# Optimization experiments

Hardware: AMD Instinct MI355X
Metric: run time of the kernel (lower is better)

Reference implementation:

```python
import jax, jax.numpy as jnp
import numpy as np

# Synthetic NEAT-style layered DAG (matches init_kwargs)
N_IN = 512      # input nodes
L = 5           # computed layers (last = outputs)
M = 2048        # nodes per computed layer
FAN = 32        # incoming edges per computed node
B = 1024        # batch size
N = N_IN + L * M        # total nodes
E = M * FAN             # edges per layer (grouped by destination layer)


def setup_inputs() -> dict:
    rng = np.random.default_rng(0)
    src = np.zeros((L, E), np.int32)
    dst = np.zeros((L, E), np.int32)
    for l in range(L):
        prefix = N_IN + l * M  # edges may come from any earlier node (DAG w/ skips)
        src[l] = rng.integers(0, prefix, size=E)
        dst[l] = np.repeat(np.arange(M, dtype=np.int32), FAN)
    key = jax.random.key(0)
    k1, k2, k3 = jax.random.split(key, 3)
    x = jax.random.normal(k1, (B, N_IN), jnp.float32)
    weights = jax.random.normal(k2, (L, E), jnp.float32) * 0.1
    biases = jax.random.normal(k3, (L, M), jnp.float32) * 0.01
    return {
        "x": x,
        "weights": weights,
        "biases": biases,
        "src_idx": jnp.asarray(src),
        "dst_idx": jnp.asarray(dst),
    }


def reference(x, weights, biases, src_idx, dst_idx):
    b = x.shape[0]
    # values[:, node] as in the torch module; inputs copied in first
    vals = jnp.zeros((b, N), x.dtype).at[:, :N_IN].set(x)
    for l in range(L):  # topological layers (fixed, small count)
        # gather source activations for this layer's edges and weight them
        contrib = vals[:, src_idx[l]] * weights[l]                    # [B, E]
        # scatter-add into destination nodes of this layer
        layer = jnp.zeros((b, M), x.dtype).at[:, dst_idx[l]].add(contrib)
        layer = jax.nn.relu(layer + biases[l])
        vals = vals.at[:, N_IN + l * M : N_IN + (l + 1) * M].set(layer)
    # output nodes = last computed layer
    return vals[:, N_IN + (L - 1) * M :]
```

## Files before the change

### kernel.cpp

```cpp
#include <hip/hip_runtime.h>

#define N_IN    512
#define NLAYERS 5
#define M_NODES 2048
#define FAN     32
#define B_BATCH 1024
#define E_EDGES (M_NODES * FAN)
#define N_TOTAL (N_IN + NLAYERS * M_NODES)
#define PREFIX4 (N_IN + 4 * M_NODES)

#define CB      4
#define NBLK    (B_BATCH / CB)
#define GROUPS  (M_NODES / 64)
#define ECH     (FAN / 4)
#define NODES_ALL (NLAYERS * M_NODES)

typedef unsigned short u16;
typedef unsigned int   u32;

__device__ __forceinline__ u16 f2bf(float f) {
    u32 b = __float_as_uint(f);
    return (u16)((b + 0x7FFFu + ((b >> 16) & 1u)) >> 16);
}

__global__ __launch_bounds__(256) void pack_edges(
    const float* __restrict__ w,
    const int* __restrict__ src,
    u32* __restrict__ pck) {
    const int n = blockIdx.x * 256 + threadIdx.x;
    if (n >= NODES_ALL) return;
    const int l = n >> 11;
    const int j = n & (M_NODES - 1);

    u32 words[FAN];
    int cnt[16];
#pragma unroll
    for (int i = 0; i < 16; ++i) cnt[i] = 0;

    const size_t eb = (size_t)l * E_EDGES + (size_t)j * FAN;
#pragma unroll 1
    for (int k = 0; k < FAN; ++k) {
        const int s = src[eb + k];
        words[k] = ((u32)f2bf(w[eb + k]) << 16) | (u32)(s & 0xFFFF);
        cnt[s & 15]++;
    }
    int startp[16];
    int acc = 0;
#pragma unroll
    for (int i = 0; i < 16; ++i) { startp[i] = acc; acc += cnt[i]; }

    const int g    = j >> 6;
    const int lane = j & 63;
    const int rot  = j & 31;
    const size_t nb = (size_t)(l * GROUPS + g) * ECH;
#pragma unroll 1
    for (int k = 0; k < FAN; ++k) {
        const u32 wd  = words[k];
        const int key = wd & 15;
        const int r   = startp[key]++;
        const int kp  = (r + rot) & 31;
        pck[((nb + (kp >> 2)) * 64 + lane) * 4 + (kp & 3)] = wd;
    }
}

__global__ __launch_bounds__(1024) void net_kernel(
    const float* __restrict__ x,
    const u32* __restrict__ pck,
    const float* __restrict__ bias,
    float* __restrict__ out) {
    __shared__ uint2 vals2[PREFIX4];

    const int t   = threadIdx.x;
    const int blk = blockIdx.x;

    if (t < N_IN) {
        const float v0 = x[(size_t)(CB * blk + 0) * N_IN + t];
        const float v1 = x[(size_t)(CB * blk + 1) * N_IN + t];
        const float v2 = x[(size_t)(CB * blk + 2) * N_IN + t];
        const float v3 = x[(size_t)(CB * blk + 3) * N_IN + t];
        vals2[t] = make_uint2((u32)f2bf(v0) | ((u32)f2bf(v1) << 16),
                              (u32)f2bf(v2) | ((u32)f2bf(v3) << 16));
    }

    for (int l = 0; l < NLAYERS; ++l) {
        __syncthreads();
        const int base = N_IN + l * M_NODES;
#pragma unroll
        for (int r = 0; r < 2; ++r) {
            const int j     = r * 1024 + t;
            const int g     = j >> 6;
            const int lane6 = j & 63;
            const uint4* ep = reinterpret_cast<const uint4*>(pck) +
                              (size_t)(l * GROUPS + g) * ECH * 64 + lane6;
            const float bj = bias[l * M_NODES + j];
            float a0 = bj, a1 = bj, a2 = bj, a3 = bj;

            uint4 wd = ep[0];
#pragma unroll
            for (int ec = 0; ec < ECH; ++ec) {
                const uint4 nxt = (ec < ECH - 1) ? ep[(ec + 1) * 64] : wd;
#pragma unroll
                for (int c = 0; c < 4; ++c) {
                    const u32 word = (c == 0) ? wd.x : (c == 1) ? wd.y
                                    : (c == 2) ? wd.z : wd.w;
                    const u32 s    = word & 0xFFFFu;
                    const float wv = __uint_as_float(word & 0xFFFF0000u);
                    const uint2 v  = vals2[s];
                    a0 = fmaf(wv, __uint_as_float(v.x << 16),          a0);
                    a1 = fmaf(wv, __uint_as_float(v.x & 0xFFFF0000u), a1);
                    a2 = fmaf(wv, __uint_as_float(v.y << 16),          a2);
                    a3 = fmaf(wv, __uint_as_float(v.y & 0xFFFF0000u), a3);
                }
                wd = nxt;
            }
            a0 = fmaxf(a0, 0.f);
            a1 = fmaxf(a1, 0.f);
            a2 = fmaxf(a2, 0.f);
            a3 = fmaxf(a3, 0.f);
            if (l < NLAYERS - 1) {
                vals2[base + j] =
                    make_uint2((u32)f2bf(a0) | ((u32)f2bf(a1) << 16),
                               (u32)f2bf(a2) | ((u32)f2bf(a3) << 16));
            } else {
                out[(size_t)(CB * blk + 0) * M_NODES + j] = a0;
                out[(size_t)(CB * blk + 1) * M_NODES + j] = a1;
                out[(size_t)(CB * blk + 2) * M_NODES + j] = a2;
                out[(size_t)(CB * blk + 3) * M_NODES + j] = a3;
            }
        }
    }
}

extern "C" void kernel_launch(void* const* d_in, const int* in_sizes, int n_in,
                              void* d_out, int out_size, void* d_ws, size_t ws_size,
                              hipStream_t stream) {
    const float* x       = (const float*)d_in[0];
    const float* weights = (const float*)d_in[1];
    const float* biases  = (const float*)d_in[2];
    const int*   src_idx = (const int*)d_in[3];
    float* out = (float*)d_out;
    u32*   pck = (u32*)d_ws;

    pack_edges<<<(NODES_ALL + 255) / 256, 256, 0, stream>>>(
        weights, src_idx, pck);

    net_kernel<<<NBLK, 1024, 0, stream>>>(x, pck, biases, out);
}
```

Before: 107.0 us.

## Rewrite edge packing as block-cooperative shared-memory sort with coalesced I/O

The edge-packing kernel now uses one 1024-thread block per 64-node group. Threads read src and weight pairs with coalesced vector loads, bucket them by source low bits using shared-memory atomics, and write the packed output fully coalesced. The old version had each thread walk its own node's 32 edges with strided loads and scattered stores. The change targets the memory inefficiency of the preprocessing kernel, at the cost of extra barriers and shared atomics. Because atomic order is nondeterministic, the ordering within each bucket may vary from run to run, but the sums stay equivalent.

```diff
diff --git a/kernel.cpp b/kernel.cpp
--- a/kernel.cpp
+++ b/kernel.cpp
@@ -23,43 +23,59 @@
     return (u16)((b + 0x7FFFu + ((b >> 16) & 1u)) >> 16);
 }
 
-__global__ __launch_bounds__(256) void pack_edges(
+__global__ __launch_bounds__(1024) void pack_edges(
     const float* __restrict__ w,
     const int* __restrict__ src,
     u32* __restrict__ pck) {
-    const int n = blockIdx.x * 256 + threadIdx.x;
-    if (n >= NODES_ALL) return;
-    const int l = n >> 11;
-    const int j = n & (M_NODES - 1);
+    __shared__ u32 s_word[2048];
+    __shared__ u32 s_sorted[64][32];
+    __shared__ int s_cnt[64][16];
+    __shared__ int s_start[64][16];
 
-    u32 words[FAN];
-    int cnt[16];
+    const int t  = threadIdx.x;
+    const int lg = blockIdx.x;
+    const size_t ebase = (size_t)lg * 2048;
+
+    if (t < 64 * 16) ((int*)s_cnt)[t] = 0;
+    __syncthreads();
+
+    const int e0 = t * 2;
+    const int node = e0 >> 5;
+    const int2   s2 = *reinterpret_cast<const int2*>(src + ebase + e0);
+    const float2 w2 = *reinterpret_cast<const float2*>(w + ebase + e0);
+    const u32 wd0 = ((u32)f2bf(w2.x) << 16) | (u32)(s2.x & 0xFFFF);
+    const u32 wd1 = ((u32)f2bf(w2.y) << 16) | (u32)(s2.y & 0xFFFF);
+    s_word[e0]     = wd0;
+    s_word[e0 + 1] = wd1;
+    atomicAdd(&s_cnt[node][s2.x & 15], 1);
+    atomicAdd(&s_cnt[node][s2.y & 15], 1);
+    __syncthreads();
+
+    if (t < 64) {
+        int acc = 0;
 #pragma unroll
-    for (int i = 0; i < 16; ++i) cnt[i] = 0;
+        for (int i = 0; i < 16; ++i) {
+            s_start[t][i] = acc;
+            acc += s_cnt[t][i];
+        }
+    }
+    __syncthreads();
 
-    const size_t eb = (size_t)l * E_EDGES + (size_t)j * FAN;
-#pragma unroll 1
-    for (int k = 0; k < FAN; ++k) {
-        const int s = src[eb + k];
-        words[k] = ((u32)f2bf(w[eb + k]) << 16) | (u32)(s & 0xFFFF);
-        cnt[s & 15]++;
+    const int rot = node & 31;
+    {
+        const int r0 = atomicAdd(&s_start[node][wd0 & 15], 1);
+        s_sorted[node][(r0 + rot) & 31] = wd0;
+        const int r1 = atomicAdd(&s_start[node][wd1 & 15], 1);
+        s_sorted[node][(r1 + rot) & 31] = wd1;
     }
-    int startp[16];
-    int acc = 0;
+    __syncthreads();
+
 #pragma unroll
-    for (int i = 0; i < 16; ++i) { startp[i] = acc; acc += cnt[i]; }
-
-    const int g    = j >> 6;
-    const int lane = j & 63;
-    const int rot  = j & 31;
-    const size_t nb = (size_t)(l * GROUPS + g) * ECH;
-#pragma unroll 1
-    for (int k = 0; k < FAN; ++k) {
-        const u32 wd  = words[k];
-        const int key = wd & 15;
-        const int r   = startp[key]++;
-        const int kp  = (r + rot) & 31;
-        pck[((nb + (kp >> 2)) * 64 + lane) * 4 + (kp & 3)] = wd;
+    for (int i = 0; i < 2; ++i) {
+        const int p    = t + i * 1024;
+        const int lane = (p >> 2) & 63;
+        const int kp   = ((p >> 8) << 2) | (p & 3);
+        pck[ebase + p] = s_sorted[lane][kp];
     }
 }
 
@@ -141,8 +157,7 @@
     float* out = (float*)d_out;
     u32*   pck = (u32*)d_ws;
 
-    pack_edges<<<(NODES_ALL + 255) / 256, 256, 0, stream>>>(
-        weights, src_idx, pck);
+    pack_edges<<<NLAYERS * GROUPS, 1024, 0, stream>>>(weights, src_idx, pck);
 
     net_kernel<<<NBLK, 1024, 0, stream>>>(x, pck, biases, out);
 }
```

Measured after the change: 90.32 us. -15.6%, faster.

## Parallelize edge packing per edge, use packed FMA and batched LDS gathers

Applied to the files above, without the earlier changes.

The pack kernel now gives each edge its own thread instead of looping per node, and it drops the bank-conflict-avoiding sort and rotation of edges by source low bits. The main kernel issues all four LDS gathers of a chunk before the FMAs. It also uses two-wide float vector FMAs, which can map to packed FP32 instructions on CDNA3/4. The aim is to cut the serial pack cost and the ALU instruction count, but removing the bank-aware ordering may bring back LDS bank conflicts in the gather.

```diff
diff --git a/kernel.cpp b/kernel.cpp
--- a/kernel.cpp
+++ b/kernel.cpp
@@ -13,54 +13,30 @@
 #define NBLK    (B_BATCH / CB)
 #define GROUPS  (M_NODES / 64)
 #define ECH     (FAN / 4)
-#define NODES_ALL (NLAYERS * M_NODES)
 
 typedef unsigned short u16;
 typedef unsigned int   u32;
+typedef __attribute__((ext_vector_type(2))) float f32x2;
 
 __device__ __forceinline__ u16 f2bf(float f) {
     u32 b = __float_as_uint(f);
     return (u16)((b + 0x7FFFu + ((b >> 16) & 1u)) >> 16);
 }
 
-__global__ __launch_bounds__(256) void pack_edges(
+__global__ __launch_bounds__(1024) void pack_edges(
     const float* __restrict__ w,
     const int* __restrict__ src,
     u32* __restrict__ pck) {
-    const int n = blockIdx.x * 256 + threadIdx.x;
-    if (n >= NODES_ALL) return;
-    const int l = n >> 11;
-    const int j = n & (M_NODES - 1);
-
-    u32 words[FAN];
-    int cnt[16];
-#pragma unroll
-    for (int i = 0; i < 16; ++i) cnt[i] = 0;
-
-    const size_t eb = (size_t)l * E_EDGES + (size_t)j * FAN;
-#pragma unroll 1
-    for (int k = 0; k < FAN; ++k) {
-        const int s = src[eb + k];
-        words[k] = ((u32)f2bf(w[eb + k]) << 16) | (u32)(s & 0xFFFF);
-        cnt[s & 15]++;
-    }
-    int startp[16];
-    int acc = 0;
-#pragma unroll
-    for (int i = 0; i < 16; ++i) { startp[i] = acc; acc += cnt[i]; }
-
+    const int e = blockIdx.x * 1024 + threadIdx.x;
+    const int l    = e >> 16;
+    const int j    = (e >> 5) & (M_NODES - 1);
+    const int k    = e & (FAN - 1);
     const int g    = j >> 6;
     const int lane = j & 63;
-    const int rot  = j & 31;
-    const size_t nb = (size_t)(l * GROUPS + g) * ECH;
-#pragma unroll 1
-    for (int k = 0; k < FAN; ++k) {
-        const u32 wd  = words[k];
-        const int key = wd & 15;
-        const int r   = startp[key]++;
-        const int kp  = (r + rot) & 31;
-        pck[((nb + (kp >> 2)) * 64 + lane) * 4 + (kp & 3)] = wd;
-    }
+    const int ec   = k >> 2;
+    const int c    = k & 3;
+    const u32 word = ((u32)f2bf(w[e]) << 16) | (u32)(src[e] & 0xFFFF);
+    pck[((((l * GROUPS + g) * ECH + ec) * 64) + lane) * 4 + c] = word;
 }
 
 __global__ __launch_bounds__(1024) void net_kernel(
@@ -82,41 +58,47 @@
                               (u32)f2bf(v2) | ((u32)f2bf(v3) << 16));
     }
 
+    const int g0    = t >> 6;
+    const int lane6 = t & 63;
+
     for (int l = 0; l < NLAYERS; ++l) {
         __syncthreads();
         const int base = N_IN + l * M_NODES;
 #pragma unroll
         for (int r = 0; r < 2; ++r) {
-            const int j     = r * 1024 + t;
-            const int g     = j >> 6;
-            const int lane6 = j & 63;
+            const int j = r * 1024 + t;
             const uint4* ep = reinterpret_cast<const uint4*>(pck) +
-                              (size_t)(l * GROUPS + g) * ECH * 64 + lane6;
+                              (size_t)(l * GROUPS + g0 + r * 16) * ECH * 64 +
+                              lane6;
             const float bj = bias[l * M_NODES + j];
-            float a0 = bj, a1 = bj, a2 = bj, a3 = bj;
+            f32x2 a01 = {bj, bj};
+            f32x2 a23 = {bj, bj};
 
             uint4 wd = ep[0];
 #pragma unroll
             for (int ec = 0; ec < ECH; ++ec) {
                 const uint4 nxt = (ec < ECH - 1) ? ep[(ec + 1) * 64] : wd;
+                const u32 ew[4] = {wd.x, wd.y, wd.z, wd.w};
+                uint2 v[4];
+#pragma unroll
+                for (int c = 0; c < 4; ++c) v[c] = vals2[ew[c] & 0xFFFFu];
 #pragma unroll
                 for (int c = 0; c < 4; ++c) {
-                    const u32 word = (c == 0) ? wd.x : (c == 1) ? wd.y
-                                    : (c == 2) ? wd.z : wd.w;
-                    const u32 s    = word & 0xFFFFu;
-                    const float wv = __uint_as_float(word & 0xFFFF0000u);
-                    const uint2 v  = vals2[s];
-                    a0 = fmaf(wv, __uint_as_float(v.x << 16),          a0);
-                    a1 = fmaf(wv, __uint_as_float(v.x & 0xFFFF0000u), a1);
-                    a2 = fmaf(wv, __uint_as_float(v.y << 16),          a2);
-                    a3 = fmaf(wv, __uint_as_float(v.y & 0xFFFF0000u), a3);
+                    const float wv = __uint_as_float(ew[c] & 0xFFFF0000u);
+                    const f32x2 w2 = {wv, wv};
+                    const f32x2 p01 = {__uint_as_float(v[c].x << 16),
+                                       __uint_as_float(v[c].x & 0xFFFF0000u)};
+                    const f32x2 p23 = {__uint_as_float(v[c].y << 16),
+                                       __uint_as_float(v[c].y & 0xFFFF0000u)};
+                    a01 = __builtin_elementwise_fma(w2, p01, a01);
+                    a23 = __builtin_elementwise_fma(w2, p23, a23);
                 }
                 wd = nxt;
             }
-            a0 = fmaxf(a0, 0.f);
-            a1 = fmaxf(a1, 0.f);
-            a2 = fmaxf(a2, 0.f);
-            a3 = fmaxf(a3, 0.f);
+            const float a0 = fmaxf(a01[0], 0.f);
+            const float a1 = fmaxf(a01[1], 0.f);
+            const float a2 = fmaxf(a23[0], 0.f);
+            const float a3 = fmaxf(a23[1], 0.f);
             if (l < NLAYERS - 1) {
                 vals2[base + j] =
                     make_uint2((u32)f2bf(a0) | ((u32)f2bf(a1) << 16),
@@ -141,7 +123,7 @@
     float* out = (float*)d_out;
     u32*   pck = (u32*)d_ws;
 
-    pack_edges<<<(NODES_ALL + 255) / 256, 256, 0, stream>>>(
+    pack_edges<<<NLAYERS * E_EDGES / 1024, 1024, 0, stream>>>(
         weights, src_idx, pck);
 
     net_kernel<<<NBLK, 1024, 0, stream>>>(x, pck, biases, out);
```

New measurement: 94.29 us. 11.9% less time.
